# Kernel optimization log

Hardware: AMD Instinct MI355X
Metric: run time of the kernel (lower is better)

## Reference

```python
import jax, jax.numpy as jnp
import numpy as np

N_HEADS = 12

def setup_inputs() -> dict:
    key = jax.random.key(0)
    k1, k2, k3 = jax.random.split(key, 3)
    B, L, D = 2, 2048, 768
    x = jax.random.normal(k1, (B, L, D), dtype=jnp.float32)
    attention_mask = jnp.ones((B, L), dtype=jnp.int32)  # 1 = real token
    w_qkv = jax.random.normal(k2, (D, 3 * D), dtype=jnp.float32) * (1.0 / np.sqrt(D))
    b_qkv = jnp.zeros((3 * D,), dtype=jnp.float32)
    w_out = jax.random.normal(k3, (D, D), dtype=jnp.float32) * (1.0 / np.sqrt(D))
    b_out = jnp.zeros((D,), dtype=jnp.float32)
    return {"x": x, "attention_mask": attention_mask, "w_qkv": w_qkv,
            "b_qkv": b_qkv, "w_out": w_out, "b_out": b_out}

def reference(x, attention_mask, w_qkv, b_qkv, w_out, b_out):
    B, L, D = x.shape
    H = N_HEADS
    dk = D // H
    # fused QKV projection
    qkv = jnp.einsum('bld,de->ble', x, w_qkv) + b_qkv  # (B,L,3D)
    q, k, v = jnp.split(qkv, 3, axis=-1)
    def to_heads(t):
        return t.reshape(B, L, H, dk).transpose(0, 2, 1, 3)  # (B,H,L,dk)
    q, k, v = to_heads(q), to_heads(k), to_heads(v)
    scale = 1.0 / jnp.sqrt(jnp.asarray(dk, dtype=x.dtype))
    scores = jnp.einsum('bhqd,bhkd->bhqk', q, k) * scale  # (B,H,L,L)
    mask = (attention_mask != 0)[:, None, None, :]  # (B,1,1,L), True = keep
    neg = jnp.asarray(jnp.finfo(scores.dtype).min, dtype=scores.dtype)
    scores = jnp.where(mask, scores, neg)
    weights = jax.nn.softmax(scores, axis=-1)
    out = jnp.einsum('bhqk,bhkd->bhqd', weights, v)  # (B,H,L,dk)
    out = out.transpose(0, 2, 1, 3).reshape(B, L, D)
    return jnp.einsum('bld,de->ble', out, w_out) + b_out
```

## Files before the change

kernel.cpp:

```cpp
#include <hip/hip_runtime.h>

typedef __bf16 bf16;
typedef bf16 bf16x4 __attribute__((ext_vector_type(4)));
typedef bf16 bf16x8 __attribute__((ext_vector_type(8)));
typedef float f32x4 __attribute__((ext_vector_type(4)));

#define MFMA16(A, B, C) __builtin_amdgcn_mfma_f32_16x16x32_bf16(A, B, C, 0, 0, 0)
#define NEG_BIG -30000.0f

#define GLOAD_LDS16(gptr, lptr)                                                \
    __builtin_amdgcn_global_load_lds(                                          \
        (__attribute__((address_space(1))) void*)(gptr),                       \
        (__attribute__((address_space(3))) void*)(lptr), 16, 0, 0)

#define SW(r, c8) ((r) * 64 + (((((c8) >> 3) ^ ((r) & 7))) << 3))
#define SW32(r, q) ((r) * 32 + ((((q) ^ ((r) & 3))) << 3))

__global__ void mark_k(float* __restrict__ out, float val, int n) {
    int i = blockIdx.x * 256 + threadIdx.x;
    if (i < n) out[i] = val;
}

__global__ __launch_bounds__(256) void cvt_x_k(const float* __restrict__ src,
                                               bf16* __restrict__ dst, int n) {
    int i = (blockIdx.x * 256 + threadIdx.x) * 8;
    if (i >= n) return;
    float4 a = *(const float4*)&src[i];
    float4 b = *(const float4*)&src[i + 4];
    bf16x8 w;
    w[0] = (bf16)a.x; w[1] = (bf16)a.y; w[2] = (bf16)a.z; w[3] = (bf16)a.w;
    w[4] = (bf16)b.x; w[5] = (bf16)b.y; w[6] = (bf16)b.z; w[7] = (bf16)b.w;
    *(bf16x8*)&dst[i] = w;
}

__global__ __launch_bounds__(256) void transpose_cvt_tiled(
    const float* __restrict__ src, bf16* __restrict__ dst, int R, int C) {
    __shared__ float t[32][33];
    int tid = threadIdx.x, tx = tid & 31, ty = tid >> 5;
    int bx = blockIdx.x * 32, by = blockIdx.y * 32;
#pragma unroll
    for (int i = 0; i < 4; ++i) {
        int row = by + ty + i * 8;
        t[ty + i * 8][tx] = src[(size_t)row * C + bx + tx];
    }
    __syncthreads();
#pragma unroll
    for (int i = 0; i < 4; ++i) {
        int outrow = bx + ty + i * 8;
        dst[(size_t)outrow * R + by + tx] = (bf16)t[tx][ty + i * 8];
    }
}

#define CLD 136

__global__ __launch_bounds__(256) void gemm_qkv_v6(
    const bf16* __restrict__ A, const bf16* __restrict__ B,
    const float* __restrict__ bias, bf16* __restrict__ Qh,
    bf16* __restrict__ Kh, bf16* __restrict__ Vth) {
    __shared__ __align__(16) bf16 SMEM[128 * CLD];
    int tid = threadIdx.x, lane = tid & 63, wave = tid >> 6;
    int quad = lane >> 4, l16 = lane & 15;
    int wr = wave >> 1, wc = wave & 1;
    int t = ((blockIdx.x & 7) * 72) + (blockIdx.x >> 3);
    int bx = t % 18, by = t / 18;
    int m0 = by * 128, n0 = bx * 128;
    const int K = 768;
    const f32x4 fz = {0.f, 0.f, 0.f, 0.f};
    f32x4 acc[4][4];
#pragma unroll
    for (int nj = 0; nj < 4; ++nj)
#pragma unroll
        for (int mi = 0; mi < 4; ++mi) acc[nj][mi] = fz;
    const bf16* Ablk = A + (size_t)m0 * K;
    const bf16* Bblk = B + (size_t)n0 * K;
    int srow = lane >> 2, c = lane & 3;

    auto stage = [&](int kn, int d) {
#pragma unroll
        for (int i = 0; i < 2; ++i) {
            int r0 = i * 64 + wave * 16;
            int row = r0 + srow;
            int sc = (c ^ (row & 3)) << 3;
            GLOAD_LDS16(&Ablk[(size_t)row * K + kn + sc],
                        &SMEM[d * 8192 + r0 * 32]);
            GLOAD_LDS16(&Bblk[(size_t)row * K + kn + sc],
                        &SMEM[4096 + d * 8192 + r0 * 32]);
        }
    };
    stage(0, 0);

    auto body = [&](int k0, int P) {
        __syncthreads();
        if (k0 + 32 < K) stage(k0 + 32, P ^ 1);
        const bf16* Asp = &SMEM[P * 8192];
        const bf16* Bsp = &SMEM[4096 + P * 8192];
        bf16x8 af[4], bfv[4];
#pragma unroll
        for (int tt = 0; tt < 4; ++tt) {
            af[tt]  = *(const bf16x8*)&Asp[SW32(wr * 64 + tt * 16 + l16, quad)];
            bfv[tt] = *(const bf16x8*)&Bsp[SW32(wc * 64 + tt * 16 + l16, quad)];
        }
#pragma unroll
        for (int nj = 0; nj < 4; ++nj)
#pragma unroll
            for (int mi = 0; mi < 4; ++mi)
                acc[nj][mi] = MFMA16(bfv[nj], af[mi], acc[nj][mi]);
    };
    for (int k0 = 0; k0 < K; k0 += 64) { body(k0, 0); body(k0 + 32, 1); }

    int which = n0 / 768;
    int h0 = (n0 % 768) >> 6;
    int b = m0 >> 11, l0 = m0 & 2047;
    __syncthreads();

    if (which == 2) {
#pragma unroll
        for (int nj = 0; nj < 4; ++nj) {
            int cl0 = wc * 64 + nj * 16 + quad * 4;
            float4 bv4 = *(const float4*)&bias[n0 + cl0];
            float bv[4] = {bv4.x, bv4.y, bv4.z, bv4.w};
#pragma unroll
            for (int mi = 0; mi < 4; ++mi) {
                int xrl = wr * 64 + mi * 16 + l16;
#pragma unroll
                for (int r = 0; r < 4; ++r)
                    SMEM[(cl0 + r) * CLD + xrl] = (bf16)(acc[nj][mi][r] + bv[r]);
            }
        }
    } else {
        float s = (which == 0) ? 0.18033688f : 1.0f;
#pragma unroll
        for (int nj = 0; nj < 4; ++nj) {
            int cl0 = wc * 64 + nj * 16 + quad * 4;
            float4 bv4 = *(const float4*)&bias[n0 + cl0];
            float bv[4] = {bv4.x, bv4.y, bv4.z, bv4.w};
#pragma unroll
            for (int mi = 0; mi < 4; ++mi) {
                int xrl = wr * 64 + mi * 16 + l16;
                bf16x4 v;
#pragma unroll
                for (int r = 0; r < 4; ++r) v[r] = (bf16)((acc[nj][mi][r] + bv[r]) * s);
                *(bf16x4*)&SMEM[xrl * CLD + cl0] = v;
            }
        }
    }
    __syncthreads();

    if (which == 2) {
#pragma unroll
        for (int i = 0; i < 8; ++i) {
            int idx = i * 256 + tid;
            int cl = idx >> 4, ch = idx & 15;
            int d = cl & 63, h = h0 + (cl >> 6);
            bf16x8 v = *(const bf16x8*)&SMEM[cl * CLD + ch * 8];
            *(bf16x8*)&Vth[((size_t)(b * 12 + h) * 64 + d) * 2048 + l0 + ch * 8] = v;
        }
    } else {
        bf16* dst = (which == 0) ? Qh : Kh;
#pragma unroll
        for (int i = 0; i < 8; ++i) {
            int idx = i * 256 + tid;
            int rr = idx >> 4, ch = idx & 15;
            int h = h0 + (ch >> 3), d0 = (ch & 7) * 8;
            bf16x8 v = *(const bf16x8*)&SMEM[rr * CLD + ch * 8];
            *(bf16x8*)&dst[((size_t)(b * 12 + h) * 2048 + l0 + rr) * 64 + d0] = v;
        }
    }
}

__global__ __launch_bounds__(256) void gemm_out_v5(
    const bf16* __restrict__ A, const bf16* __restrict__ B,
    const float* __restrict__ bias, float* __restrict__ C) {
    __shared__ __align__(16) bf16 As[2][64 * 32];
    __shared__ __align__(16) bf16 Bs[2][128 * 32];
    int tid = threadIdx.x, lane = tid & 63, wave = tid >> 6;
    int quad = lane >> 4, l16 = lane & 15;
    int wr = wave >> 1, wc = wave & 1;
    int t = ((blockIdx.x & 7) * 48) + (blockIdx.x >> 3);
    int bx = t % 6, by = t / 6;
    int m0 = by * 64, n0 = bx * 128;
    const int K = 768, N = 768;
    const f32x4 fz = {0.f, 0.f, 0.f, 0.f};
    f32x4 acc[2][4];
#pragma unroll
    for (int mi = 0; mi < 2; ++mi)
#pragma unroll
        for (int nj = 0; nj < 4; ++nj) acc[mi][nj] = fz;
    const bf16* Ablk = A + (size_t)m0 * K;
    const bf16* Bblk = B + (size_t)n0 * K;
    int srow = lane >> 2, c = lane & 3;

    auto stage = [&](int kn, int d) {
        {
            int r0 = wave * 16;
            int row = r0 + srow;
            int sc = (c ^ (row & 3)) << 3;
            GLOAD_LDS16(&Ablk[(size_t)row * K + kn + sc], &As[d][r0 * 32]);
        }
#pragma unroll
        for (int i = 0; i < 2; ++i) {
            int r0 = i * 64 + wave * 16;
            int row = r0 + srow;
            int sc = (c ^ (row & 3)) << 3;
            GLOAD_LDS16(&Bblk[(size_t)row * K + kn + sc], &Bs[d][r0 * 32]);
        }
    };
    stage(0, 0);

    auto body = [&](int k0, int P) {
        __syncthreads();
        if (k0 + 32 < K) stage(k0 + 32, P ^ 1);
        bf16x8 af[2], bfv[4];
#pragma unroll
        for (int tt = 0; tt < 2; ++tt)
            af[tt] = *(const bf16x8*)&As[P][SW32(wr * 32 + tt * 16 + l16, quad)];
#pragma unroll
        for (int tt = 0; tt < 4; ++tt)
            bfv[tt] = *(const bf16x8*)&Bs[P][SW32(wc * 64 + tt * 16 + l16, quad)];
#pragma unroll
        for (int mi = 0; mi < 2; ++mi)
#pragma unroll
            for (int nj = 0; nj < 4; ++nj)
                acc[mi][nj] = MFMA16(af[mi], bfv[nj], acc[mi][nj]);
    };
    for (int k0 = 0; k0 < K; k0 += 64) { body(k0, 0); body(k0 + 32, 1); }

#pragma unroll
    for (int nj = 0; nj < 4; ++nj) {
        int col = n0 + wc * 64 + nj * 16 + l16;
        float bv = bias[col];
#pragma unroll
        for (int mi = 0; mi < 2; ++mi)
#pragma unroll
            for (int r = 0; r < 4; ++r) {
                int row = m0 + wr * 32 + mi * 16 + quad * 4 + r;
                C[(size_t)row * N + col] = acc[mi][nj][r] + bv;
            }
    }
}

__global__ __launch_bounds__(256) void flash_attn(
    const bf16* __restrict__ Q, const bf16* __restrict__ K,
    const bf16* __restrict__ V, const int* __restrict__ mask,
    bf16* __restrict__ po0, bf16* __restrict__ po1, float* __restrict__ lbuf) {
    __shared__ __align__(16) bf16 Ks[2][64 * 64];
    __shared__ __align__(16) bf16 Vs[2][64 * 64];
    __shared__ float maskS[1024];
    __shared__ int cleanF;

    int tid = threadIdx.x, lane = tid & 63, wave = tid >> 6;
    int quad = lane >> 4, l16 = lane & 15;

    int n = blockIdx.x;
    int xcd = n & 7, idx = n >> 3;
    int g = xcd * 6 + (idx >> 4);
    int m = idx & 15;
    int bh = g % 24;
    int split = g / 24;
    int b = bh / 12;
    int s0 = split * 1024;
    int q0 = m * 128 + wave * 32;

    bf16x8 aq[2][2];
#pragma unroll
    for (int qt = 0; qt < 2; ++qt) {
        const bf16* Qp = Q + ((size_t)bh * 2048 + q0 + qt * 16 + l16) * 64;
        aq[qt][0] = *(const bf16x8*)(Qp + quad * 8);
        aq[qt][1] = *(const bf16x8*)(Qp + 32 + quad * 8);
    }

    if (tid == 0) cleanF = 1;
    __syncthreads();
    const int* mrow = mask + b * 2048 + s0;
    int myclean = 1;
#pragma unroll
    for (int i = 0; i < 4; ++i) {
        int idx2 = i * 256 + tid;
        int mv = mrow[idx2];
        maskS[idx2] = mv ? 0.0f : NEG_BIG;
        myclean &= (mv != 0);
    }
    if (!myclean) cleanF = 0;

    const f32x4 fz = {0.f, 0.f, 0.f, 0.f};
    f32x4 o[2][4];
    float l_i[2] = {0.f, 0.f};
#pragma unroll
    for (int qt = 0; qt < 2; ++qt)
#pragma unroll
        for (int dt = 0; dt < 4; ++dt) o[qt][dt] = fz;

    int srow = tid >> 3;
    int sc8  = (tid & 7) * 8;
    const bf16* Kbase = K + ((size_t)bh * 2048 + s0) * 64;
    const bf16* Vbase = V + (size_t)bh * 64 * 2048 + s0;

#pragma unroll
    for (int i = 0; i < 2; ++i) {
        int row = srow + i * 32;
        *(bf16x8*)&Ks[0][SW(row, sc8)] =
            *(const bf16x8*)&Kbase[(size_t)row * 64 + sc8];
        *(bf16x8*)&Vs[0][SW(row, sc8)] =
            *(const bf16x8*)&Vbase[(size_t)row * 2048 + sc8];
    }
    __syncthreads();
    int clean = cleanF;

    auto body = [&](int kb, int P) {
        bf16x8 kreg[2], vreg[2];
        const bool pref = (kb + 64 < 1024);
        if (pref) {
            int nb = kb + 64;
#pragma unroll
            for (int i = 0; i < 2; ++i) {
                int row = srow + i * 32;
                kreg[i] = *(const bf16x8*)&Kbase[(size_t)(nb + row) * 64 + sc8];
                vreg[i] = *(const bf16x8*)&Vbase[(size_t)row * 2048 + nb + sc8];
            }
        }

        __builtin_amdgcn_s_setprio(1);
        f32x4 s[2][4];
#pragma unroll
        for (int ct = 0; ct < 4; ++ct) {
            int krow = ct * 16 + l16;
            bf16x8 kf0 = *(const bf16x8*)&Ks[P][SW(krow, quad * 8)];
            bf16x8 kf1 = *(const bf16x8*)&Ks[P][SW(krow, 32 + quad * 8)];
#pragma unroll
            for (int qt = 0; qt < 2; ++qt) {
                f32x4 tt = fz;
                tt = MFMA16(kf0, aq[qt][0], tt);
                tt = MFMA16(kf1, aq[qt][1], tt);
                s[qt][ct] = tt;
            }
        }

        if (!clean) {
#pragma unroll
            for (int ct = 0; ct < 4; ++ct) {
                float4 mv = *(const float4*)&maskS[kb + ct * 16 + quad * 4];
                float ma[4] = {mv.x, mv.y, mv.z, mv.w};
#pragma unroll
                for (int qt = 0; qt < 2; ++qt)
#pragma unroll
                    for (int r = 0; r < 4; ++r) s[qt][ct][r] += ma[r];
            }
        }

        bf16x8 vf[2][4];
#pragma unroll
        for (int ks = 0; ks < 2; ++ks)
#pragma unroll
            for (int dt = 0; dt < 4; ++dt)
                vf[ks][dt] =
                    *(const bf16x8*)&Vs[P][SW(dt * 16 + l16, ks * 32 + quad * 8)];

#pragma unroll
        for (int qt = 0; qt < 2; ++qt) {
#pragma unroll
            for (int ct = 0; ct < 4; ++ct)
#pragma unroll
                for (int r = 0; r < 4; ++r)
                    s[qt][ct][r] = __builtin_amdgcn_exp2f(s[qt][ct][r]);
            float t0 = (s[qt][0][0] + s[qt][0][1]) + (s[qt][0][2] + s[qt][0][3]);
            float t1 = (s[qt][1][0] + s[qt][1][1]) + (s[qt][1][2] + s[qt][1][3]);
            float t2 = (s[qt][2][0] + s[qt][2][1]) + (s[qt][2][2] + s[qt][2][3]);
            float t3 = (s[qt][3][0] + s[qt][3][1]) + (s[qt][3][2] + s[qt][3][3]);
            l_i[qt] += (t0 + t1) + (t2 + t3);

            unsigned pk0[4], pk1[4];
#pragma unroll
            for (int ct = 0; ct < 4; ++ct) {
                asm("v_cvt_pk_bf16_f32 %0, %1, %2"
                    : "=v"(pk0[ct]) : "v"(s[qt][ct][0]), "v"(s[qt][ct][1]));
                asm("v_cvt_pk_bf16_f32 %0, %1, %2"
                    : "=v"(pk1[ct]) : "v"(s[qt][ct][2]), "v"(s[qt][ct][3]));
            }

#pragma unroll
            for (int ks = 0; ks < 2; ++ks) {
                unsigned a0 = pk0[2 * ks], c0 = pk0[2 * ks + 1];
                unsigned b0 = pk1[2 * ks], d0 = pk1[2 * ks + 1];
                asm("v_permlane32_swap_b32 %0, %1" : "+v"(a0), "+v"(c0));
                asm("v_permlane16_swap_b32 %0, %1" : "+v"(a0), "+v"(c0));
                asm("v_permlane32_swap_b32 %0, %1" : "+v"(b0), "+v"(d0));
                asm("v_permlane16_swap_b32 %0, %1" : "+v"(b0), "+v"(d0));
                union { unsigned u[4]; bf16x8 v; } ap;
                ap.u[0] = a0;
                ap.u[1] = b0;
                ap.u[2] = c0;
                ap.u[3] = d0;
#pragma unroll
                for (int dt = 0; dt < 4; ++dt)
                    o[qt][dt] = MFMA16(ap.v, vf[ks][dt], o[qt][dt]);
            }
        }
        __builtin_amdgcn_s_setprio(0);

        if (pref) {
#pragma unroll
            for (int i = 0; i < 2; ++i) {
                int row = srow + i * 32;
                *(bf16x8*)&Ks[P ^ 1][SW(row, sc8)] = kreg[i];
                *(bf16x8*)&Vs[P ^ 1][SW(row, sc8)] = vreg[i];
            }
        }
        __syncthreads();
    };

    for (int kb = 0; kb < 1024; kb += 128) { body(kb, 0); body(kb + 64, 1); }

    int h = bh % 12;
    bf16* obase = split ? po1 : po0;
#pragma unroll
    for (int qt = 0; qt < 2; ++qt) {
        l_i[qt] += __shfl_xor(l_i[qt], 16);
        l_i[qt] += __shfl_xor(l_i[qt], 32);
#pragma unroll
        for (int dt = 0; dt < 4; ++dt)
#pragma unroll
            for (int r = 0; r < 4; ++r) {
                int qrow = q0 + qt * 16 + quad * 4 + r;
                obase[((size_t)b * 2048 + qrow) * 768 + h * 64 + dt * 16 + l16] =
                    (bf16)o[qt][dt][r];
            }
        if (quad == 0) {
            int qrow = q0 + qt * 16 + l16;
            lbuf[((size_t)split * 24 + bh) * 2048 + qrow] = l_i[qt];
        }
    }
}

__global__ __launch_bounds__(256) void merge_k(
    bf16* __restrict__ ctx, const bf16* __restrict__ po1,
    const float* __restrict__ lbuf) {
    int idx = blockIdx.x * 256 + threadIdx.x;
    if (idx >= 4096 * 768 / 8) return;
    size_t i8 = (size_t)idx * 8;
    int row = (int)(i8 / 768);
    int col = (int)(i8 % 768);
    int bh = (row >> 11) * 12 + (col >> 6);
    int qrow = row & 2047;
    float l0 = lbuf[(size_t)bh * 2048 + qrow];
    float l1 = lbuf[(size_t)(24 + bh) * 2048 + qrow];
    float inv = 1.0f / (l0 + l1);
    bf16x8 v0 = *(const bf16x8*)&ctx[i8];
    bf16x8 v1 = *(const bf16x8*)&po1[i8];
    bf16x8 o;
#pragma unroll
    for (int k = 0; k < 8; ++k)
        o[k] = (bf16)(((float)v0[k] + (float)v1[k]) * inv);
    *(bf16x8*)&ctx[i8] = o;
}

extern "C" void kernel_launch(void* const* d_in, const int* in_sizes, int n_in,
                              void* d_out, int out_size, void* d_ws, size_t ws_size,
                              hipStream_t stream) {
    float* out = (float*)d_out;

    const float* x = nullptr; const int* mask = nullptr;
    const float* w_qkv = nullptr; const float* b_qkv = nullptr;
    const float* w_out = nullptr; const float* b_out = nullptr;
    int found = 0;
    for (int i = 0; i < n_in; ++i) {
        switch (in_sizes[i]) {
            case 3145728: x     = (const float*)d_in[i]; found |= 1;  break;
            case 4096:    mask  = (const int*)  d_in[i]; found |= 2;  break;
            case 1769472: w_qkv = (const float*)d_in[i]; found |= 4;  break;
            case 2304:    b_qkv = (const float*)d_in[i]; found |= 8;  break;
            case 589824:  w_out = (const float*)d_in[i]; found |= 16; break;
            case 768:     b_out = (const float*)d_in[i]; found |= 32; break;
        }
    }
    if (found != 63) {
        mark_k<<<(out_size + 255) / 256, 256, 0, stream>>>(
            out, 200.0f + (float)found, out_size);
        return;
    }

    const int M = 4096, D = 768, N3 = 2304;
    const size_t HEADS_ELEMS = (size_t)24 * 2048 * 64;

    bf16* ws    = (bf16*)d_ws;
    bf16* Kh    = ws;
    bf16* Vth   = Kh + HEADS_ELEMS;
    bf16* ctx   = Vth + HEADS_ELEMS;
    bf16* wqkvT = ctx + (size_t)M * D;
    bf16* woutT = wqkvT + (size_t)N3 * D;
    bf16* Qh    = (bf16*)d_out;
    bf16* xb    = (bf16*)d_out + HEADS_ELEMS;
    bf16* po1   = xb;
    float* lbuf = (float*)wqkvT;

    cvt_x_k<<<(M * D / 8 + 255) / 256, 256, 0, stream>>>(x, xb, M * D);
    transpose_cvt_tiled<<<dim3(2304 / 32, 768 / 32), 256, 0, stream>>>(
        w_qkv, wqkvT, 768, 2304);
    transpose_cvt_tiled<<<dim3(768 / 32, 768 / 32), 256, 0, stream>>>(
        w_out, woutT, 768, 768);

    gemm_qkv_v6<<<dim3(576), 256, 0, stream>>>(
        xb, wqkvT, b_qkv, Qh, Kh, Vth);

    flash_attn<<<dim3(768), 256, 0, stream>>>(
        Qh, Kh, Vth, mask, ctx, po1, lbuf);

    merge_k<<<(4096 * 768 / 8 + 255) / 256, 256, 0, stream>>>(ctx, po1, lbuf);

    gemm_out_v5<<<dim3(384), 256, 0, stream>>>(
        ctx, woutT, b_out, out);
}
```

Before: 174.7 us.

## Fuse split-K merge into output GEMM and merge prep kernels into one launch

Three prep kernels (x conversion plus two weight transposes) become a single launch with block-range dispatch. The merge kernel, which combined the two attention halves and normalized by the softmax sums, is removed. Its work now happens in the output GEMM's A-tile staging, which loads both partials, scales them by per-row inverse sums precomputed into LDS, and writes to LDS through registers instead of async global-to-LDS loads. The flash-attention loop also drops its s_setprio hints and changes from a two-step unrolled lambda to a plain loop with a toggled buffer index. This saves two launches and one full round trip of the context tensor, at the cost of synchronous A loads in the GEMM.

Result: faster. 170.8 us (median of 3 runs) (-2.2%).

```diff
diff --git a/kernel.cpp b/kernel.cpp
--- a/kernel.cpp
+++ b/kernel.cpp
@@ -21,33 +21,44 @@
     if (i < n) out[i] = val;
 }
 
-__global__ __launch_bounds__(256) void cvt_x_k(const float* __restrict__ src,
-                                               bf16* __restrict__ dst, int n) {
-    int i = (blockIdx.x * 256 + threadIdx.x) * 8;
-    if (i >= n) return;
-    float4 a = *(const float4*)&src[i];
-    float4 b = *(const float4*)&src[i + 4];
-    bf16x8 w;
-    w[0] = (bf16)a.x; w[1] = (bf16)a.y; w[2] = (bf16)a.z; w[3] = (bf16)a.w;
-    w[4] = (bf16)b.x; w[5] = (bf16)b.y; w[6] = (bf16)b.z; w[7] = (bf16)b.w;
-    *(bf16x8*)&dst[i] = w;
-}
-
-__global__ __launch_bounds__(256) void transpose_cvt_tiled(
-    const float* __restrict__ src, bf16* __restrict__ dst, int R, int C) {
+__global__ __launch_bounds__(256) void prep_k(
+    const float* __restrict__ x, bf16* __restrict__ xb,
+    const float* __restrict__ w_qkv, bf16* __restrict__ wqkvT,
+    const float* __restrict__ w_out, bf16* __restrict__ woutT) {
     __shared__ float t[32][33];
+    int blk = blockIdx.x;
+    if (blk < 1536) {
+        int i = (blk * 256 + threadIdx.x) * 8;
+        float4 a = *(const float4*)&x[i];
+        float4 b = *(const float4*)&x[i + 4];
+        bf16x8 w;
+        w[0] = (bf16)a.x; w[1] = (bf16)a.y; w[2] = (bf16)a.z; w[3] = (bf16)a.w;
+        w[4] = (bf16)b.x; w[5] = (bf16)b.y; w[6] = (bf16)b.z; w[7] = (bf16)b.w;
+        *(bf16x8*)&xb[i] = w;
+        return;
+    }
+    blk -= 1536;
+    const float* src; bf16* dst; int R, C, bx, by;
+    if (blk < 1728) {
+        src = w_qkv; dst = wqkvT; R = 768; C = 2304;
+        bx = blk % 72; by = blk / 72;
+    } else {
+        blk -= 1728;
+        src = w_out; dst = woutT; R = 768; C = 768;
+        bx = blk % 24; by = blk / 24;
+    }
     int tid = threadIdx.x, tx = tid & 31, ty = tid >> 5;
-    int bx = blockIdx.x * 32, by = blockIdx.y * 32;
+    int x0 = bx * 32, y0 = by * 32;
 #pragma unroll
     for (int i = 0; i < 4; ++i) {
-        int row = by + ty + i * 8;
-        t[ty + i * 8][tx] = src[(size_t)row * C + bx + tx];
+        int row = y0 + ty + i * 8;
+        t[ty + i * 8][tx] = src[(size_t)row * C + x0 + tx];
     }
     __syncthreads();
 #pragma unroll
     for (int i = 0; i < 4; ++i) {
-        int outrow = bx + ty + i * 8;
-        dst[(size_t)outrow * R + by + tx] = (bf16)t[tx][ty + i * 8];
+        int outrow = x0 + ty + i * 8;
+        dst[(size_t)outrow * R + y0 + tx] = (bf16)t[tx][ty + i * 8];
     }
 }
 
@@ -168,11 +179,13 @@
     }
 }
 
-__global__ __launch_bounds__(256) void gemm_out_v5(
-    const bf16* __restrict__ A, const bf16* __restrict__ B,
+__global__ __launch_bounds__(256) void gemm_out_v6(
+    const bf16* __restrict__ po0, const bf16* __restrict__ po1,
+    const float* __restrict__ lbuf, const bf16* __restrict__ B,
     const float* __restrict__ bias, float* __restrict__ C) {
     __shared__ __align__(16) bf16 As[2][64 * 32];
     __shared__ __align__(16) bf16 Bs[2][128 * 32];
+    __shared__ float inv_s[768];
     int tid = threadIdx.x, lane = tid & 63, wave = tid >> 6;
     int quad = lane >> 4, l16 = lane & 15;
     int wr = wave >> 1, wc = wave & 1;
@@ -180,23 +193,44 @@
     int bx = t % 6, by = t / 6;
     int m0 = by * 64, n0 = bx * 128;
     const int K = 768, N = 768;
+    int b = m0 >> 11;
+
+#pragma unroll
+    for (int j = 0; j < 3; ++j) {
+        int idx = j * 256 + tid;
+        int r = idx & 63, h = idx >> 6;
+        int qrow = (m0 + r) & 2047;
+        int bh = b * 12 + h;
+        float l0 = lbuf[(size_t)bh * 2048 + qrow];
+        float l1 = lbuf[(size_t)(24 + bh) * 2048 + qrow];
+        inv_s[idx] = 1.0f / (l0 + l1);
+    }
+    __syncthreads();
+
     const f32x4 fz = {0.f, 0.f, 0.f, 0.f};
     f32x4 acc[2][4];
 #pragma unroll
     for (int mi = 0; mi < 2; ++mi)
 #pragma unroll
         for (int nj = 0; nj < 4; ++nj) acc[mi][nj] = fz;
-    const bf16* Ablk = A + (size_t)m0 * K;
     const bf16* Bblk = B + (size_t)n0 * K;
     int srow = lane >> 2, c = lane & 3;
 
-    auto stage = [&](int kn, int d) {
-        {
-            int r0 = wave * 16;
-            int row = r0 + srow;
-            int sc = (c ^ (row & 3)) << 3;
-            GLOAD_LDS16(&Ablk[(size_t)row * K + kn + sc], &As[d][r0 * 32]);
-        }
+    auto stageA = [&](int kn, int d) {
+        int row = wave * 16 + srow;
+        int sc = (c ^ (row & 3)) << 3;
+        int col = kn + sc;
+        float inv = inv_s[(col >> 6) * 64 + row];
+        size_t gi = (size_t)(m0 + row) * 768 + col;
+        bf16x8 a0 = *(const bf16x8*)&po0[gi];
+        bf16x8 a1 = *(const bf16x8*)&po1[gi];
+        bf16x8 w;
+#pragma unroll
+        for (int k = 0; k < 8; ++k)
+            w[k] = (bf16)(((float)a0[k] + (float)a1[k]) * inv);
+        *(bf16x8*)&As[d][row * 32 + c * 8] = w;
+    };
+    auto stageB = [&](int kn, int d) {
 #pragma unroll
         for (int i = 0; i < 2; ++i) {
             int r0 = i * 64 + wave * 16;
@@ -205,11 +239,12 @@
             GLOAD_LDS16(&Bblk[(size_t)row * K + kn + sc], &Bs[d][r0 * 32]);
         }
     };
-    stage(0, 0);
+    stageA(0, 0);
+    stageB(0, 0);
 
     auto body = [&](int k0, int P) {
         __syncthreads();
-        if (k0 + 32 < K) stage(k0 + 32, P ^ 1);
+        if (k0 + 32 < K) { stageA(k0 + 32, P ^ 1); stageB(k0 + 32, P ^ 1); }
         bf16x8 af[2], bfv[4];
 #pragma unroll
         for (int tt = 0; tt < 2; ++tt)
@@ -306,9 +341,10 @@
     __syncthreads();
     int clean = cleanF;
 
-    auto body = [&](int kb, int P) {
+    int p = 0;
+    for (int kb = 0; kb < 1024; kb += 64) {
         bf16x8 kreg[2], vreg[2];
-        const bool pref = (kb + 64 < 1024);
+        const int pref = (kb + 64 < 1024);
         if (pref) {
             int nb = kb + 64;
 #pragma unroll
@@ -319,19 +355,18 @@
             }
         }
 
-        __builtin_amdgcn_s_setprio(1);
         f32x4 s[2][4];
 #pragma unroll
         for (int ct = 0; ct < 4; ++ct) {
             int krow = ct * 16 + l16;
-            bf16x8 kf0 = *(const bf16x8*)&Ks[P][SW(krow, quad * 8)];
-            bf16x8 kf1 = *(const bf16x8*)&Ks[P][SW(krow, 32 + quad * 8)];
+            bf16x8 kf0 = *(const bf16x8*)&Ks[p][SW(krow, quad * 8)];
+            bf16x8 kf1 = *(const bf16x8*)&Ks[p][SW(krow, 32 + quad * 8)];
 #pragma unroll
             for (int qt = 0; qt < 2; ++qt) {
-                f32x4 tt = fz;
-                tt = MFMA16(kf0, aq[qt][0], tt);
-                tt = MFMA16(kf1, aq[qt][1], tt);
-                s[qt][ct] = tt;
+                f32x4 t = fz;
+                t = MFMA16(kf0, aq[qt][0], t);
+                t = MFMA16(kf1, aq[qt][1], t);
+                s[qt][ct] = t;
             }
         }
 
@@ -352,8 +387,7 @@
         for (int ks = 0; ks < 2; ++ks)
 #pragma unroll
             for (int dt = 0; dt < 4; ++dt)
-                vf[ks][dt] =
-                    *(const bf16x8*)&Vs[P][SW(dt * 16 + l16, ks * 32 + quad * 8)];
+                vf[ks][dt] = *(const bf16x8*)&Vs[p][SW(dt * 16 + l16, ks * 32 + quad * 8)];
 
 #pragma unroll
         for (int qt = 0; qt < 2; ++qt) {
@@ -395,20 +429,18 @@
                     o[qt][dt] = MFMA16(ap.v, vf[ks][dt], o[qt][dt]);
             }
         }
-        __builtin_amdgcn_s_setprio(0);
 
         if (pref) {
 #pragma unroll
             for (int i = 0; i < 2; ++i) {
                 int row = srow + i * 32;
-                *(bf16x8*)&Ks[P ^ 1][SW(row, sc8)] = kreg[i];
-                *(bf16x8*)&Vs[P ^ 1][SW(row, sc8)] = vreg[i];
+                *(bf16x8*)&Ks[1 - p][SW(row, sc8)] = kreg[i];
+                *(bf16x8*)&Vs[1 - p][SW(row, sc8)] = vreg[i];
             }
         }
         __syncthreads();
-    };
-
-    for (int kb = 0; kb < 1024; kb += 128) { body(kb, 0); body(kb + 64, 1); }
+        p ^= 1;
+    }
 
     int h = bh % 12;
     bf16* obase = split ? po1 : po0;
@@ -429,28 +461,6 @@
             lbuf[((size_t)split * 24 + bh) * 2048 + qrow] = l_i[qt];
         }
     }
-}
-
-__global__ __launch_bounds__(256) void merge_k(
-    bf16* __restrict__ ctx, const bf16* __restrict__ po1,
-    const float* __restrict__ lbuf) {
-    int idx = blockIdx.x * 256 + threadIdx.x;
-    if (idx >= 4096 * 768 / 8) return;
-    size_t i8 = (size_t)idx * 8;
-    int row = (int)(i8 / 768);
-    int col = (int)(i8 % 768);
-    int bh = (row >> 11) * 12 + (col >> 6);
-    int qrow = row & 2047;
-    float l0 = lbuf[(size_t)bh * 2048 + qrow];
-    float l1 = lbuf[(size_t)(24 + bh) * 2048 + qrow];
-    float inv = 1.0f / (l0 + l1);
-    bf16x8 v0 = *(const bf16x8*)&ctx[i8];
-    bf16x8 v1 = *(const bf16x8*)&po1[i8];
-    bf16x8 o;
-#pragma unroll
-    for (int k = 0; k < 8; ++k)
-        o[k] = (bf16)(((float)v0[k] + (float)v1[k]) * inv);
-    *(bf16x8*)&ctx[i8] = o;
 }
 
 extern "C" void kernel_launch(void* const* d_in, const int* in_sizes, int n_in,
@@ -484,28 +494,23 @@
     bf16* ws    = (bf16*)d_ws;
     bf16* Kh    = ws;
     bf16* Vth   = Kh + HEADS_ELEMS;
-    bf16* ctx   = Vth + HEADS_ELEMS;
-    bf16* wqkvT = ctx + (size_t)M * D;
+    bf16* po0   = Vth + HEADS_ELEMS;
+    bf16* wqkvT = po0 + (size_t)M * D;
     bf16* woutT = wqkvT + (size_t)N3 * D;
+    bf16* po1   = woutT + (size_t)D * D;
     bf16* Qh    = (bf16*)d_out;
     bf16* xb    = (bf16*)d_out + HEADS_ELEMS;
-    bf16* po1   = xb;
     float* lbuf = (float*)wqkvT;
 
-    cvt_x_k<<<(M * D / 8 + 255) / 256, 256, 0, stream>>>(x, xb, M * D);
-    transpose_cvt_tiled<<<dim3(2304 / 32, 768 / 32), 256, 0, stream>>>(
-        w_qkv, wqkvT, 768, 2304);
-    transpose_cvt_tiled<<<dim3(768 / 32, 768 / 32), 256, 0, stream>>>(
-        w_out, woutT, 768, 768);
+    prep_k<<<dim3(1536 + 1728 + 576), 256, 0, stream>>>(
+        x, xb, w_qkv, wqkvT, w_out, woutT);
 
     gemm_qkv_v6<<<dim3(576), 256, 0, stream>>>(
         xb, wqkvT, b_qkv, Qh, Kh, Vth);
 
     flash_attn<<<dim3(768), 256, 0, stream>>>(
-        Qh, Kh, Vth, mask, ctx, po1, lbuf);
-
-    merge_k<<<(4096 * 768 / 8 + 255) / 256, 256, 0, stream>>>(ctx, po1, lbuf);
-
-    gemm_out_v5<<<dim3(384), 256, 0, stream>>>(
-        ctx, woutT, b_out, out);
+        Qh, Kh, Vth, mask, po0, po1, lbuf);
+
+    gemm_out_v6<<<dim3(384), 256, 0, stream>>>(
+        po0, po1, lbuf, woutT, b_out, out);
 }
```
